# Kernel tuning notes

Measured on AMD Instinct MI355X. Metric: run time of the kernel, lower is better.

Reference implementation:

```python
import jax, jax.numpy as jnp
import numpy as np

ACT_BITS = 8  # global_act_bit in the original repo
QMAX = float(2 ** ACT_BITS - 1)


def _fake_quant_asym(x):
    """Asymmetric per-tensor fake quantization (weight_quant_fn, activate=True)."""
    mx = jnp.max(x)
    mn = jnp.min(x)
    scale = (mx - mn) / QMAX
    zp = jnp.round(-mn / scale)
    q = jnp.clip(jnp.round(x / scale) + zp, 0.0, QMAX)
    return (q - zp) * scale


def setup_inputs() -> dict:
    key = jax.random.key(0)
    kx, kq, kr, kl, ks = jax.random.split(key, 5)
    B, S, IN, OUT, R = 32, 1024, 1152, 1152, 64
    x = jax.random.normal(kx, (B, S, IN), dtype=jnp.float32)
    quant_w = jax.random.normal(kq, (OUT, IN), dtype=jnp.float32) * 0.02  # quant.weight
    right_w = jax.random.normal(kr, (R, IN), dtype=jnp.float32) * 0.02   # right.weight
    left_w = jax.random.normal(kl, (OUT, R), dtype=jnp.float32) * 0.02   # left.weight
    bias = jnp.zeros((OUT,), dtype=jnp.float32)
    scales = jax.random.uniform(ks, (IN,), dtype=jnp.float32, minval=0.5, maxval=2.0)
    return {"x": x, "quant_w": quant_w, "right_w": right_w,
            "left_w": left_w, "bias": bias, "scales": scales}


def reference(x, quant_w, right_w, left_w, bias, scales):
    # inference path, merge=False: smooth-quant style scale division, then
    # asymmetric per-tensor fake quant, then quant GEMM + low-rank SVD adapter.
    xs = x / scales                                   # [B,S,IN] elementwise
    xq = _fake_quant_asym(xs)                         # global max/min fake quant
    hx = jnp.einsum('bsi,oi->bso', xq, quant_w)       # quantized linear
    lrx = jnp.einsum('bsr,or->bso',
                     jnp.einsum('bsi,ri->bsr', xq, right_w), left_w)  # low-rank
    return hx + lrx + bias
```

## Files before the change

kernel.cpp:

```cpp
#include <hip/hip_runtime.h>
#include <hip/hip_bf16.h>
#include <stdint.h>

#define M_DIM   32768
#define IN_DIM  1152
#define OUT_DIM 1152
#define R_DIM   64
#define QMAXF   255.0f

#define RED_BLOCKS 4096
#define QBLOCKS    4096

typedef float  f32x4  __attribute__((ext_vector_type(4)));
typedef __bf16 bf16x8 __attribute__((ext_vector_type(8)));

static __device__ __forceinline__ unsigned short f2bf(float f) {
    unsigned int u = __float_as_uint(f);
    unsigned int r = (u + 0x7fffu + ((u >> 16) & 1u)) >> 16;
    return (unsigned short)r;
}

__global__ __launch_bounds__(256) void k_minmax(const float* __restrict__ x,
                                                const float* __restrict__ scales,
                                                float* __restrict__ partials) {
    const int n4 = (M_DIM * IN_DIM) / 4;
    int tid = blockIdx.x * 256 + threadIdx.x;
    const int stride = RED_BLOCKS * 256;
    float mn = 3.4e38f, mx = -3.4e38f;
    for (int i4 = tid; i4 < n4; i4 += stride) {
        int i = i4 * 4;
        float4 xv = *(const float4*)(x + i);
        int c = i % IN_DIM;
        float4 sv = *(const float4*)(scales + c);
        float a0 = xv.x / sv.x, a1 = xv.y / sv.y;
        float a2 = xv.z / sv.z, a3 = xv.w / sv.w;
        mn = fminf(mn, fminf(fminf(a0, a1), fminf(a2, a3)));
        mx = fmaxf(mx, fmaxf(fmaxf(a0, a1), fmaxf(a2, a3)));
    }
    #pragma unroll
    for (int off = 32; off > 0; off >>= 1) {
        mn = fminf(mn, __shfl_down(mn, off));
        mx = fmaxf(mx, __shfl_down(mx, off));
    }
    __shared__ float smn[4], smx[4];
    int lane = threadIdx.x & 63, wv = threadIdx.x >> 6;
    if (lane == 0) { smn[wv] = mn; smx[wv] = mx; }
    __syncthreads();
    if (threadIdx.x == 0) {
        float bmn = fminf(fminf(smn[0], smn[1]), fminf(smn[2], smn[3]));
        float bmx = fmaxf(fmaxf(smx[0], smx[1]), fmaxf(smx[2], smx[3]));
        partials[blockIdx.x * 2]     = bmn;
        partials[blockIdx.x * 2 + 1] = bmx;
    }
}

__global__ __launch_bounds__(256) void k_finalize(const float* __restrict__ partials,
                                                  float* __restrict__ qp) {
    float mn = 3.4e38f, mx = -3.4e38f;
    for (int i = threadIdx.x; i < RED_BLOCKS; i += 256) {
        mn = fminf(mn, partials[i * 2]);
        mx = fmaxf(mx, partials[i * 2 + 1]);
    }
    #pragma unroll
    for (int off = 32; off > 0; off >>= 1) {
        mn = fminf(mn, __shfl_down(mn, off));
        mx = fmaxf(mx, __shfl_down(mx, off));
    }
    __shared__ float smn[4], smx[4];
    int lane = threadIdx.x & 63, wv = threadIdx.x >> 6;
    if (lane == 0) { smn[wv] = mn; smx[wv] = mx; }
    __syncthreads();
    if (threadIdx.x == 0) {
        float bmn = fminf(fminf(smn[0], smn[1]), fminf(smn[2], smn[3]));
        float bmx = fmaxf(fmaxf(smx[0], smx[1]), fmaxf(smx[2], smx[3]));
        float qs = (bmx - bmn) / QMAXF;
        float zp = rintf(-bmn / qs);
        qp[0] = qs;
        qp[1] = zp;
    }
}

__global__ __launch_bounds__(256) void k_quant(const float* __restrict__ x,
                                               const float* __restrict__ scales,
                                               const float* __restrict__ qp,
                                               unsigned short* __restrict__ xq) {
    const float qs = qp[0], zp = qp[1];
    const int n4 = (M_DIM * IN_DIM) / 4;
    int tid = blockIdx.x * 256 + threadIdx.x;
    const int stride = QBLOCKS * 256;
    for (int i4 = tid; i4 < n4; i4 += stride) {
        int i = i4 * 4;
        float4 xv = *(const float4*)(x + i);
        int c = i % IN_DIM;
        float4 sv = *(const float4*)(scales + c);
        float a[4] = { xv.x / sv.x, xv.y / sv.y, xv.z / sv.z, xv.w / sv.w };
        ushort4 o;
        unsigned short* op = (unsigned short*)&o;
        #pragma unroll
        for (int j = 0; j < 4; j++) {
            float q = rintf(a[j] / qs) + zp;
            q = fminf(fmaxf(q, 0.0f), QMAXF);
            op[j] = f2bf(q - zp);
        }
        *(ushort4*)(xq + i) = o;
    }
}

__global__ __launch_bounds__(256) void k_wprep(const float* __restrict__ qw,
                                               const float* __restrict__ rw,
                                               const float* __restrict__ lw,
                                               unsigned short* __restrict__ wc) {
    int idx = blockIdx.x * 256 + threadIdx.x;
    int o = idx / IN_DIM;
    int i = idx - o * IN_DIM;
    float acc = qw[idx];
    #pragma unroll 8
    for (int r = 0; r < R_DIM; r++)
        acc += lw[o * R_DIM + r] * rw[r * IN_DIM + i];
    wc[idx] = f2bf(acc);
}

#define BM 128
#define BN 128
#define BK 32

__global__ __launch_bounds__(256) void k_gemm(const unsigned short* __restrict__ A,
                                              const unsigned short* __restrict__ Bw,
                                              const float* __restrict__ bias,
                                              const float* __restrict__ qp,
                                              float* __restrict__ C) {
    __shared__ __align__(16) unsigned short As[BM * BK];
    __shared__ __align__(16) unsigned short Bs[BN * BK];
    const int tid = threadIdx.x;
    const int bm = blockIdx.x, bn = blockIdx.y;
    const int K = IN_DIM, N = OUT_DIM;

    const int r0 = tid >> 2;
    const int c0 = (tid & 3) * 8;
    const unsigned short* ga0 = A  + (size_t)(bm * BM + r0) * K + c0;
    const unsigned short* ga1 = ga0 + (size_t)64 * K;
    const unsigned short* gb0 = Bw + (size_t)(bn * BN + r0) * K + c0;
    const unsigned short* gb1 = gb0 + (size_t)64 * K;
    unsigned short* lA0 = As + tid * 8;
    unsigned short* lA1 = As + tid * 8 + 2048;
    unsigned short* lB0 = Bs + tid * 8;
    unsigned short* lB1 = Bs + tid * 8 + 2048;

    f32x4 acc[4][4];
    #pragma unroll
    for (int mi = 0; mi < 4; mi++)
        #pragma unroll
        for (int ni = 0; ni < 4; ni++)
            acc[mi][ni] = (f32x4)0.0f;

    const int lane = tid & 63, wv = tid >> 6;
    const int wm = (wv & 1) * 64;
    const int wn = (wv >> 1) * 64;
    const int l16 = lane & 15, l4 = lane >> 4;
    const bf16x8* Asv = (const bf16x8*)As;
    const bf16x8* Bsv = (const bf16x8*)Bs;
    const int afo = (wm + l16) * 4 + l4;
    const int bfo = (wn + l16) * 4 + l4;

    for (int k0 = 0; k0 < K; k0 += BK) {
        __builtin_amdgcn_global_load_lds(
            (const __attribute__((address_space(1))) unsigned int*)(ga0 + k0),
            (__attribute__((address_space(3))) unsigned int*)lA0, 16, 0, 0);
        __builtin_amdgcn_global_load_lds(
            (const __attribute__((address_space(1))) unsigned int*)(ga1 + k0),
            (__attribute__((address_space(3))) unsigned int*)lA1, 16, 0, 0);
        __builtin_amdgcn_global_load_lds(
            (const __attribute__((address_space(1))) unsigned int*)(gb0 + k0),
            (__attribute__((address_space(3))) unsigned int*)lB0, 16, 0, 0);
        __builtin_amdgcn_global_load_lds(
            (const __attribute__((address_space(1))) unsigned int*)(gb1 + k0),
            (__attribute__((address_space(3))) unsigned int*)lB1, 16, 0, 0);
        __syncthreads();

        bf16x8 af[4], bf[4];
        #pragma unroll
        for (int mi = 0; mi < 4; mi++) af[mi] = Asv[afo + mi * 64];
        #pragma unroll
        for (int ni = 0; ni < 4; ni++) bf[ni] = Bsv[bfo + ni * 64];
        #pragma unroll
        for (int mi = 0; mi < 4; mi++)
            #pragma unroll
            for (int ni = 0; ni < 4; ni++)
                acc[mi][ni] = __builtin_amdgcn_mfma_f32_16x16x32_bf16(
                    af[mi], bf[ni], acc[mi][ni], 0, 0, 0);
        __syncthreads();
    }

    const float qs = qp[0];
    #pragma unroll
    for (int mi = 0; mi < 4; mi++) {
        int row0 = bm * BM + wm + mi * 16 + l4 * 4;
        #pragma unroll
        for (int ni = 0; ni < 4; ni++) {
            int col = bn * BN + wn + ni * 16 + l16;
            float bv = bias[col];
            #pragma unroll
            for (int r = 0; r < 4; r++)
                C[(size_t)(row0 + r) * N + col] = acc[mi][ni][r] * qs + bv;
        }
    }
}

extern "C" void kernel_launch(void* const* d_in, const int* in_sizes, int n_in,
                              void* d_out, int out_size, void* d_ws, size_t ws_size,
                              hipStream_t stream) {
    const float* x      = (const float*)d_in[0];
    const float* qw     = (const float*)d_in[1];
    const float* rw     = (const float*)d_in[2];
    const float* lw     = (const float*)d_in[3];
    const float* bias   = (const float*)d_in[4];
    const float* scales = (const float*)d_in[5];

    char* ws = (char*)d_ws;
    unsigned short* xq = (unsigned short*)ws;
    unsigned short* wc = (unsigned short*)(ws + 75497472);
    float* partials    = (float*)(ws + 75497472 + 2654208);
    float* qp          = (float*)(ws + 75497472 + 2654208 + 32768);

    k_minmax  <<<RED_BLOCKS, 256, 0, stream>>>(x, scales, partials);
    k_finalize<<<1,          256, 0, stream>>>(partials, qp);
    k_quant   <<<QBLOCKS,    256, 0, stream>>>(x, scales, qp, xq);
    k_wprep   <<<(OUT_DIM * IN_DIM) / 256, 256, 0, stream>>>(qw, rw, lw, wc);

    dim3 grid(M_DIM / BM, OUT_DIM / BN);
    k_gemm<<<grid, 256, 0, stream>>>(xq, wc, bias, qp, (float*)d_out);
}
```

Measured before the change: 421.8 us.

## Restructure quantization prep with atomic min/max, reciprocal scales and row-blocked passes

Replaces the partials-plus-finalize reduction with per-block atomicMin/atomicMax on order-preserving uint encodings, which drops one kernel launch and the partials buffer. The 1/scales reciprocals are computed once in the weight-prep kernel, so the min/max and quant passes multiply instead of dividing. Both elementwise passes now work on 16-row blocks with a constant column-offset table, avoiding the per-element modulo, and use 8-wide loads and stores. Quant parameters are recomputed from the atomics in the quant and GEMM kernels. Multiplying by a reciprocal can differ from true division by one ulp, which could occasionally flip a rounding decision.

```diff
diff --git a/kernel.cpp b/kernel.cpp
--- a/kernel.cpp
+++ b/kernel.cpp
@@ -8,11 +8,13 @@
 #define R_DIM   64
 #define QMAXF   255.0f
 
-#define RED_BLOCKS 4096
-#define QBLOCKS    4096
+#define SBLOCKS     2048
+#define ROWS_PER_BLK 16
+#define CHUNKS_PER_THREAD 9
 
 typedef float  f32x4  __attribute__((ext_vector_type(4)));
 typedef __bf16 bf16x8 __attribute__((ext_vector_type(8)));
+typedef unsigned short u16x8 __attribute__((ext_vector_type(8)));
 
 static __device__ __forceinline__ unsigned short f2bf(float f) {
     unsigned int u = __float_as_uint(f);
@@ -20,97 +22,27 @@
     return (unsigned short)r;
 }
 
-__global__ __launch_bounds__(256) void k_minmax(const float* __restrict__ x,
-                                                const float* __restrict__ scales,
-                                                float* __restrict__ partials) {
-    const int n4 = (M_DIM * IN_DIM) / 4;
-    int tid = blockIdx.x * 256 + threadIdx.x;
-    const int stride = RED_BLOCKS * 256;
-    float mn = 3.4e38f, mx = -3.4e38f;
-    for (int i4 = tid; i4 < n4; i4 += stride) {
-        int i = i4 * 4;
-        float4 xv = *(const float4*)(x + i);
-        int c = i % IN_DIM;
-        float4 sv = *(const float4*)(scales + c);
-        float a0 = xv.x / sv.x, a1 = xv.y / sv.y;
-        float a2 = xv.z / sv.z, a3 = xv.w / sv.w;
-        mn = fminf(mn, fminf(fminf(a0, a1), fminf(a2, a3)));
-        mx = fmaxf(mx, fmaxf(fmaxf(a0, a1), fmaxf(a2, a3)));
-    }
-    #pragma unroll
-    for (int off = 32; off > 0; off >>= 1) {
-        mn = fminf(mn, __shfl_down(mn, off));
-        mx = fmaxf(mx, __shfl_down(mx, off));
-    }
-    __shared__ float smn[4], smx[4];
-    int lane = threadIdx.x & 63, wv = threadIdx.x >> 6;
-    if (lane == 0) { smn[wv] = mn; smx[wv] = mx; }
-    __syncthreads();
-    if (threadIdx.x == 0) {
-        float bmn = fminf(fminf(smn[0], smn[1]), fminf(smn[2], smn[3]));
-        float bmx = fmaxf(fmaxf(smx[0], smx[1]), fmaxf(smx[2], smx[3]));
-        partials[blockIdx.x * 2]     = bmn;
-        partials[blockIdx.x * 2 + 1] = bmx;
-    }
-}
-
-__global__ __launch_bounds__(256) void k_finalize(const float* __restrict__ partials,
-                                                  float* __restrict__ qp) {
-    float mn = 3.4e38f, mx = -3.4e38f;
-    for (int i = threadIdx.x; i < RED_BLOCKS; i += 256) {
-        mn = fminf(mn, partials[i * 2]);
-        mx = fmaxf(mx, partials[i * 2 + 1]);
-    }
-    #pragma unroll
-    for (int off = 32; off > 0; off >>= 1) {
-        mn = fminf(mn, __shfl_down(mn, off));
-        mx = fmaxf(mx, __shfl_down(mx, off));
-    }
-    __shared__ float smn[4], smx[4];
-    int lane = threadIdx.x & 63, wv = threadIdx.x >> 6;
-    if (lane == 0) { smn[wv] = mn; smx[wv] = mx; }
-    __syncthreads();
-    if (threadIdx.x == 0) {
-        float bmn = fminf(fminf(smn[0], smn[1]), fminf(smn[2], smn[3]));
-        float bmx = fmaxf(fmaxf(smx[0], smx[1]), fmaxf(smx[2], smx[3]));
-        float qs = (bmx - bmn) / QMAXF;
-        float zp = rintf(-bmn / qs);
-        qp[0] = qs;
-        qp[1] = zp;
-    }
-}
-
-__global__ __launch_bounds__(256) void k_quant(const float* __restrict__ x,
-                                               const float* __restrict__ scales,
-                                               const float* __restrict__ qp,
-                                               unsigned short* __restrict__ xq) {
-    const float qs = qp[0], zp = qp[1];
-    const int n4 = (M_DIM * IN_DIM) / 4;
-    int tid = blockIdx.x * 256 + threadIdx.x;
-    const int stride = QBLOCKS * 256;
-    for (int i4 = tid; i4 < n4; i4 += stride) {
-        int i = i4 * 4;
-        float4 xv = *(const float4*)(x + i);
-        int c = i % IN_DIM;
-        float4 sv = *(const float4*)(scales + c);
-        float a[4] = { xv.x / sv.x, xv.y / sv.y, xv.z / sv.z, xv.w / sv.w };
-        ushort4 o;
-        unsigned short* op = (unsigned short*)&o;
-        #pragma unroll
-        for (int j = 0; j < 4; j++) {
-            float q = rintf(a[j] / qs) + zp;
-            q = fminf(fmaxf(q, 0.0f), QMAXF);
-            op[j] = f2bf(q - zp);
-        }
-        *(ushort4*)(xq + i) = o;
-    }
-}
-
-__global__ __launch_bounds__(256) void k_wprep(const float* __restrict__ qw,
-                                               const float* __restrict__ rw,
-                                               const float* __restrict__ lw,
-                                               unsigned short* __restrict__ wc) {
+static __device__ __forceinline__ unsigned int f2ord(float f) {
+    unsigned int u = __float_as_uint(f);
+    return (u & 0x80000000u) ? ~u : (u | 0x80000000u);
+}
+static __device__ __forceinline__ float ord2f(unsigned int m) {
+    unsigned int u = (m & 0x80000000u) ? (m & 0x7fffffffu) : ~m;
+    return __uint_as_float(u);
+}
+
+__constant__ int CJ_TBL[9] = {0, 896, 640, 384, 128, 1024, 768, 512, 256};
+
+__global__ __launch_bounds__(256) void k_prep(const float* __restrict__ qw,
+                                              const float* __restrict__ rw,
+                                              const float* __restrict__ lw,
+                                              const float* __restrict__ scales,
+                                              unsigned short* __restrict__ wc,
+                                              float* __restrict__ inv_s,
+                                              unsigned int* __restrict__ qpa) {
     int idx = blockIdx.x * 256 + threadIdx.x;
+    if (idx < IN_DIM) inv_s[idx] = 1.0f / scales[idx];
+    if (idx == 0) { qpa[0] = 0xFFFFFFFFu; qpa[1] = 0u; }
     int o = idx / IN_DIM;
     int i = idx - o * IN_DIM;
     float acc = qw[idx];
@@ -120,6 +52,77 @@
     wc[idx] = f2bf(acc);
 }
 
+__global__ __launch_bounds__(256) void k_minmax(const float* __restrict__ x,
+                                                const float* __restrict__ inv_s,
+                                                unsigned int* __restrict__ qpa) {
+    const int t = threadIdx.x;
+    const size_t base = (size_t)blockIdx.x * (ROWS_PER_BLK * IN_DIM);
+    int c0 = t * 8; if (c0 >= IN_DIM) c0 -= IN_DIM;
+    float mn = 3.4e38f, mx = -3.4e38f;
+    #pragma unroll 3
+    for (int j = 0; j < CHUNKS_PER_THREAD; j++) {
+        size_t off = base + (size_t)(j * 256 + t) * 8;
+        float4 x0 = *(const float4*)(x + off);
+        float4 x1 = *(const float4*)(x + off + 4);
+        int cj = c0 + CJ_TBL[j]; if (cj >= IN_DIM) cj -= IN_DIM;
+        float4 s0 = *(const float4*)(inv_s + cj);
+        float4 s1 = *(const float4*)(inv_s + cj + 4);
+        float a0 = x0.x * s0.x, a1 = x0.y * s0.y, a2 = x0.z * s0.z, a3 = x0.w * s0.w;
+        float a4 = x1.x * s1.x, a5 = x1.y * s1.y, a6 = x1.z * s1.z, a7 = x1.w * s1.w;
+        mn = fminf(mn, fminf(fminf(fminf(a0, a1), fminf(a2, a3)),
+                             fminf(fminf(a4, a5), fminf(a6, a7))));
+        mx = fmaxf(mx, fmaxf(fmaxf(fmaxf(a0, a1), fmaxf(a2, a3)),
+                             fmaxf(fmaxf(a4, a5), fmaxf(a6, a7))));
+    }
+    #pragma unroll
+    for (int off = 32; off > 0; off >>= 1) {
+        mn = fminf(mn, __shfl_down(mn, off));
+        mx = fmaxf(mx, __shfl_down(mx, off));
+    }
+    __shared__ float smn[4], smx[4];
+    int lane = t & 63, wv = t >> 6;
+    if (lane == 0) { smn[wv] = mn; smx[wv] = mx; }
+    __syncthreads();
+    if (t == 0) {
+        float bmn = fminf(fminf(smn[0], smn[1]), fminf(smn[2], smn[3]));
+        float bmx = fmaxf(fmaxf(smx[0], smx[1]), fmaxf(smx[2], smx[3]));
+        atomicMin(&qpa[0], f2ord(bmn));
+        atomicMax(&qpa[1], f2ord(bmx));
+    }
+}
+
+__global__ __launch_bounds__(256) void k_quant(const float* __restrict__ x,
+                                               const float* __restrict__ inv_s,
+                                               const unsigned int* __restrict__ qpa,
+                                               unsigned short* __restrict__ xq) {
+    const float mn = ord2f(qpa[0]), mx = ord2f(qpa[1]);
+    const float qs = (mx - mn) / QMAXF;
+    const float zp = rintf(-mn / qs);
+    const float inv_qs = 1.0f / qs;
+    const int t = threadIdx.x;
+    const size_t base = (size_t)blockIdx.x * (ROWS_PER_BLK * IN_DIM);
+    int c0 = t * 8; if (c0 >= IN_DIM) c0 -= IN_DIM;
+    #pragma unroll 3
+    for (int j = 0; j < CHUNKS_PER_THREAD; j++) {
+        size_t off = base + (size_t)(j * 256 + t) * 8;
+        float4 x0 = *(const float4*)(x + off);
+        float4 x1 = *(const float4*)(x + off + 4);
+        int cj = c0 + CJ_TBL[j]; if (cj >= IN_DIM) cj -= IN_DIM;
+        float4 s0 = *(const float4*)(inv_s + cj);
+        float4 s1 = *(const float4*)(inv_s + cj + 4);
+        float a[8] = { x0.x * s0.x, x0.y * s0.y, x0.z * s0.z, x0.w * s0.w,
+                       x1.x * s1.x, x1.y * s1.y, x1.z * s1.z, x1.w * s1.w };
+        u16x8 o;
+        #pragma unroll
+        for (int jj = 0; jj < 8; jj++) {
+            float q = rintf(a[jj] * inv_qs) + zp;
+            q = fminf(fmaxf(q, 0.0f), QMAXF);
+            o[jj] = f2bf(q - zp);
+        }
+        *(u16x8*)(xq + off) = o;
+    }
+}
+
 #define BM 128
 #define BN 128
 #define BK 32
@@ -127,7 +130,7 @@
 __global__ __launch_bounds__(256) void k_gemm(const unsigned short* __restrict__ A,
                                               const unsigned short* __restrict__ Bw,
                                               const float* __restrict__ bias,
-                                              const float* __restrict__ qp,
+                                              const unsigned int* __restrict__ qpa,
                                               float* __restrict__ C) {
     __shared__ __align__(16) unsigned short As[BM * BK];
     __shared__ __align__(16) unsigned short Bs[BN * BK];
@@ -191,7 +194,7 @@
         __syncthreads();
     }
 
-    const float qs = qp[0];
+    const float qs = (ord2f(qpa[1]) - ord2f(qpa[0])) / QMAXF;
     #pragma unroll
     for (int mi = 0; mi < 4; mi++) {
         int row0 = bm * BM + wm + mi * 16 + l4 * 4;
@@ -219,14 +222,13 @@
     char* ws = (char*)d_ws;
     unsigned short* xq = (unsigned short*)ws;
     unsigned short* wc = (unsigned short*)(ws + 75497472);
-    float* partials    = (float*)(ws + 75497472 + 2654208);
-    float* qp          = (float*)(ws + 75497472 + 2654208 + 32768);
-
-    k_minmax  <<<RED_BLOCKS, 256, 0, stream>>>(x, scales, partials);
-    k_finalize<<<1,          256, 0, stream>>>(partials, qp);
-    k_quant   <<<QBLOCKS,    256, 0, stream>>>(x, scales, qp, xq);
-    k_wprep   <<<(OUT_DIM * IN_DIM) / 256, 256, 0, stream>>>(qw, rw, lw, wc);
+    unsigned int*  qpa = (unsigned int*)(ws + 75497472 + 2654208);
+    float* inv_s       = (float*)(ws + 75497472 + 2654208 + 16);
+
+    k_prep  <<<(OUT_DIM * IN_DIM) / 256, 256, 0, stream>>>(qw, rw, lw, scales, wc, inv_s, qpa);
+    k_minmax<<<SBLOCKS, 256, 0, stream>>>(x, inv_s, qpa);
+    k_quant <<<SBLOCKS, 256, 0, stream>>>(x, inv_s, qpa, xq);
 
     dim3 grid(M_DIM / BM, OUT_DIM / BN);
-    k_gemm<<<grid, 256, 0, stream>>>(xq, wc, bias, qp, (float*)d_out);
-}
+    k_gemm<<<grid, 256, 0, stream>>>(xq, wc, bias, qpa, (float*)d_out);
+}
```

New measurement: 553.4 us. 31.2% more time.
